# Kernel optimization log

Measured on AMD Instinct MI355X. Metric: run time of the kernel, lower is better.

The kernel has to match this reference:

```python
import jax, jax.numpy as jnp
import numpy as np

MULT = 1024
H = 16
HEAD = MULT // H  # 64

def _linear_params(key, h, out_f, in_f):
    k1, k2 = jax.random.split(key)
    bound = 1.0 / np.sqrt(in_f)
    W = jax.random.uniform(k1, (h, out_f, in_f), minval=-bound, maxval=bound, dtype=jnp.float32)
    b = jax.random.uniform(k2, (h, out_f), minval=-bound, maxval=bound, dtype=jnp.float32)
    return W, b

def setup_inputs() -> dict:
    key = jax.random.key(0)
    ks = jax.random.split(key, 6)
    t_inp = jax.random.normal(ks[0], (32768, MULT), dtype=jnp.float32)
    lat_inp = jax.random.normal(ks[1], (32768, MULT), dtype=jnp.float32)
    Wt, bt = _linear_params(ks[2], H, HEAD, MULT)
    Wl, bl = _linear_params(ks[3], H, HEAD, MULT)
    Wv, bv = _linear_params(ks[4], H, HEAD, 2 * MULT)
    k1, k2 = jax.random.split(ks[5])
    bound = 1.0 / np.sqrt(MULT)
    Wo = jax.random.uniform(k1, (MULT, MULT), minval=-bound, maxval=bound, dtype=jnp.float32)
    bo = jax.random.uniform(k2, (MULT,), minval=-bound, maxval=bound, dtype=jnp.float32)
    return {"t_inp": t_inp, "lat_inp": lat_inp, "Wt": Wt, "bt": bt,
            "Wl": Wl, "bl": bl, "Wv": Wv, "bv": bv, "Wo": Wo, "bo": bo}

def _parallel_linear(x, W, b):
    # x: [N, in], W: [H, out, in], b: [H, out] -> [N, out, H] (matches torch.stack dim=2)
    return jnp.einsum('ni,hoi->noh', x, W) + b.T[None, :, :]

def reference(t_inp, lat_inp, Wt, bt, Wl, bl, Wv, bv, Wo, bo):
    t_embed = _parallel_linear(t_inp, Wt, bt)                         # [N, HEAD, H]
    lat_emb = _parallel_linear(lat_inp, Wl, bl)                        # [N, HEAD, H]
    value_emb = _parallel_linear(jnp.concatenate((t_inp, lat_inp), axis=1), Wv, bv)  # [N, HEAD, H]
    att_weights = jax.nn.softmax(t_embed * lat_emb, axis=1)            # softmax over HEAD dim (dim=1)
    merged = (att_weights * value_emb).reshape(t_inp.shape)            # [N, MULT]
    return merged @ Wo.T + bo
```

## Files before the change

### kernel.cpp

```cpp
#include <hip/hip_runtime.h>
#include <stdint.h>
#include <stddef.h>


typedef _Float16 h8 __attribute__((ext_vector_type(8)));
typedef _Float16 h4 __attribute__((ext_vector_type(4)));
typedef float    f4 __attribute__((ext_vector_type(4)));

#define NROWS 32768

__device__ __forceinline__ void async_ld16(const void* g, void* s) {
  __builtin_amdgcn_global_load_lds(
      (const __attribute__((address_space(1))) uint32_t*)g,
      (__attribute__((address_space(3))) uint32_t*)s, 16, 0, 0);
}

#define MEMFENCE asm volatile("" ::: "memory")

template<int NT, int MODE>
__launch_bounds__(512, 2)
__global__ void gemm256(const _Float16* __restrict__ A, int lda,
                        const _Float16* __restrict__ B, int ldb,
                        const float* __restrict__ bias,
                        const _Float16* __restrict__ Et,
                        const _Float16* __restrict__ El,
                        _Float16* __restrict__ C16,
                        float* __restrict__ C32) {
  __shared__ char smem[131072];

  const int b  = blockIdx.x;
  const int bp = ((b & 7) << 6) | (b >> 3);
  const int row0 = (bp & 127) << 8;
  const int col0 = (bp >> 7) << 8;

  const int tid  = threadIdx.x;
  const int w    = tid >> 6;
  const int lane = tid & 63;
  const int quad = lane >> 4;
  const int l16  = lane & 15;
  const int wr   = w >> 2;
  const int wc   = w & 3;
  const int m    = l16 & 7;

  const uint32_t sw = (uint32_t)((quad ^ m) << 4);
  const uint32_t a0 = (uint32_t)(((wr << 7) + l16) << 7) + sw;
  const uint32_t b0 = 32768u + (uint32_t)(((wc << 6) + l16) << 7) + sw;

  const int grow = (w << 3) + (lane >> 3);
  const int ss   = ((lane & 7) ^ (lane >> 3)) << 3;
  const _Float16* pA[2][2];
  const _Float16* pB[2][2];
#pragma unroll
  for (int h = 0; h < 2; ++h)
#pragma unroll
    for (int q = 0; q < 2; ++q) {
      pA[h][q] = A + (size_t)(row0 + h * 128 + q * 64 + grow) * (size_t)lda + ss;
      pB[h][q] = B + (size_t)(col0 + h * 128 + q * 64 + grow) * (size_t)ldb + ss;
    }

  f4 acc[8][4];
  const f4 z = {0.f, 0.f, 0.f, 0.f};
#pragma unroll
  for (int i = 0; i < 8; ++i)
#pragma unroll
    for (int j = 0; j < 4; ++j) acc[i][j] = z;

  char* const sm = smem;
  const int woff = w << 10;

#pragma unroll
  for (int h = 0; h < 2; ++h)
#pragma unroll
    for (int q = 0; q < 2; ++q)
      async_ld16(pA[h][q], sm + h * 16384 + q * 8192 + woff);
#pragma unroll
  for (int h = 0; h < 2; ++h)
#pragma unroll
    for (int q = 0; q < 2; ++q)
      async_ld16(pB[h][q], sm + 32768 + h * 16384 + q * 8192 + woff);

  uint32_t cur = 0;
  for (int t = 0; t < NT; ++t) {
    const int tn = (t + 1 < NT) ? (t + 1) : t;
    const uint32_t nxt = cur ^ 65536u;

#pragma unroll
    for (int h = 0; h < 2; ++h)
#pragma unroll
      for (int q = 0; q < 2; ++q)
        async_ld16(pA[h][q] + tn * 64, sm + nxt + h * 16384 + q * 8192 + woff);
    asm volatile("s_waitcnt vmcnt(4)" ::: "memory");
    __builtin_amdgcn_s_barrier();
    MEMFENCE;
    {
      const uint32_t A0 = cur + a0, B0 = cur + b0;
      h8 af[8], bf[4];
#pragma unroll
      for (int i = 0; i < 8; ++i) af[i] = *(const h8*)(sm + A0 + i * 2048);
#pragma unroll
      for (int j = 0; j < 4; ++j) bf[j] = *(const h8*)(sm + B0 + j * 2048);
      __builtin_amdgcn_s_setprio(1);
#pragma unroll
      for (int i = 0; i < 8; ++i)
#pragma unroll
        for (int j = 0; j < 4; ++j)
          acc[i][j] = __builtin_amdgcn_mfma_f32_16x16x32_f16(af[i], bf[j],
                                                             acc[i][j], 0, 0, 0);
      __builtin_amdgcn_s_setprio(0);
    }
    MEMFENCE;
    __builtin_amdgcn_s_barrier();
    MEMFENCE;

#pragma unroll
    for (int h = 0; h < 2; ++h)
#pragma unroll
      for (int q = 0; q < 2; ++q)
        async_ld16(pB[h][q] + tn * 64, sm + nxt + 32768 + h * 16384 + q * 8192 + woff);
    {
      const uint32_t A1 = (cur + a0) ^ 64u, B1 = (cur + b0) ^ 64u;
      h8 af[8], bf[4];
#pragma unroll
      for (int i = 0; i < 8; ++i) af[i] = *(const h8*)(sm + A1 + i * 2048);
#pragma unroll
      for (int j = 0; j < 4; ++j) bf[j] = *(const h8*)(sm + B1 + j * 2048);
      __builtin_amdgcn_s_setprio(1);
#pragma unroll
      for (int i = 0; i < 8; ++i)
#pragma unroll
        for (int j = 0; j < 4; ++j)
          acc[i][j] = __builtin_amdgcn_mfma_f32_16x16x32_f16(af[i], bf[j],
                                                             acc[i][j], 0, 0, 0);
      __builtin_amdgcn_s_setprio(0);
    }
    MEMFENCE;
    __builtin_amdgcn_s_barrier();
    MEMFENCE;
    cur = nxt;
  }
  asm volatile("s_waitcnt vmcnt(0)" ::: "memory");

  const int cbase  = col0 + (wc << 6);
  const int rbase0 = row0 + (wr << 7) + (quad << 2);

  if constexpr (MODE == 0) {
    float bj[4];
#pragma unroll
    for (int j = 0; j < 4; ++j) bj[j] = bias[cbase + j * 16 + l16];
#pragma unroll
    for (int i = 0; i < 8; ++i)
#pragma unroll
      for (int j = 0; j < 4; ++j) {
        const size_t co = (size_t)(cbase + j * 16 + l16);
#pragma unroll
        for (int r = 0; r < 4; ++r)
          C16[(size_t)(rbase0 + i * 16 + r) * 1024 + co] =
              (_Float16)(acc[i][j][r] + bj[j]);
      }
  } else if constexpr (MODE == 2) {
    float bj[4];
#pragma unroll
    for (int j = 0; j < 4; ++j) bj[j] = bias[cbase + j * 16 + l16];
#pragma unroll
    for (int i = 0; i < 8; ++i)
#pragma unroll
      for (int j = 0; j < 4; ++j) {
        const size_t co = (size_t)(cbase + j * 16 + l16);
#pragma unroll
        for (int r = 0; r < 4; ++r)
          C32[(size_t)(rbase0 + i * 16 + r) * 1024 + co] = acc[i][j][r] + bj[j];
      }
  } else {
    float bvj[4];
#pragma unroll
    for (int j = 0; j < 4; ++j) bvj[j] = bias[cbase + j * 16 + l16];
#pragma unroll
    for (int i = 0; i < 8; ++i) {
      float pv[4][4];
      float s[4] = {0.f, 0.f, 0.f, 0.f};
      const int rb = rbase0 + i * 16;
#pragma unroll
      for (int j = 0; j < 4; ++j) {
        const size_t co = (size_t)(cbase + j * 16 + l16);
#pragma unroll
        for (int r = 0; r < 4; ++r) {
          const size_t off = (size_t)(rb + r) * 1024 + co;
          const float tv = (float)Et[off];
          const float lv = (float)El[off];
          const float p  = __expf(tv * lv);
          pv[j][r] = p * (acc[i][j][r] + bvj[j]);
          s[r] += p;
        }
      }
#pragma unroll
      for (int r = 0; r < 4; ++r) {
        s[r] += __shfl_xor(s[r], 1);
        s[r] += __shfl_xor(s[r], 2);
        s[r] += __shfl_xor(s[r], 4);
        s[r] += __shfl_xor(s[r], 8);
        s[r] = 1.0f / s[r];
      }
#pragma unroll
      for (int j = 0; j < 4; ++j) {
        const size_t co = (size_t)(cbase + j * 16 + l16);
#pragma unroll
        for (int r = 0; r < 4; ++r)
          C16[(size_t)(rb + r) * 1024 + co] = (_Float16)(pv[j][r] * s[r]);
      }
    }
  }
}

__global__ void cvt_inputs(const float4* __restrict__ t,
                           const float4* __restrict__ l,
                           h4* __restrict__ X) {
  const size_t idx = (size_t)blockIdx.x * 256 + threadIdx.x;
  const size_t n  = idx >> 8;
  const size_t k4 = idx & 255;
  const float4 a = t[idx];
  const float4 b = l[idx];
  h4 ha, hb;
  ha[0] = (_Float16)a.x; ha[1] = (_Float16)a.y;
  ha[2] = (_Float16)a.z; ha[3] = (_Float16)a.w;
  hb[0] = (_Float16)b.x; hb[1] = (_Float16)b.y;
  hb[2] = (_Float16)b.z; hb[3] = (_Float16)b.w;
  X[n * 512 + k4]       = ha;
  X[n * 512 + 256 + k4] = hb;
}

__global__ void cvt_flat(const float4* __restrict__ W, h4* __restrict__ Wp) {
  const int idx = blockIdx.x * 256 + threadIdx.x;
  const float4 v = W[idx];
  h4 hv;
  hv[0] = (_Float16)v.x; hv[1] = (_Float16)v.y;
  hv[2] = (_Float16)v.z; hv[3] = (_Float16)v.w;
  Wp[idx] = hv;
}

__global__ void cvt_wo_perm(const float* __restrict__ Wo,
                            _Float16* __restrict__ Wp) {
  const int idx = blockIdx.x * 256 + threadIdx.x;
  const int j = idx >> 10, c = idx & 1023;
  const int k = (c & 63) * 16 + (c >> 6);
  Wp[idx] = (_Float16)Wo[j * 1024 + k];
}

extern "C" void kernel_launch(void* const* d_in, const int* in_sizes, int n_in,
                              void* d_out, int out_size, void* d_ws, size_t ws_size,
                              hipStream_t stream) {
  const float* t_inp = (const float*)d_in[0];
  const float* l_inp = (const float*)d_in[1];
  const float* Wt = (const float*)d_in[2];
  const float* bt = (const float*)d_in[3];
  const float* Wl = (const float*)d_in[4];
  const float* bl = (const float*)d_in[5];
  const float* Wv = (const float*)d_in[6];
  const float* bv = (const float*)d_in[7];
  const float* Wo = (const float*)d_in[8];
  const float* bo = (const float*)d_in[9];
  float* out = (float*)d_out;

  char* ws = (char*)d_ws;
  _Float16* X16  = (_Float16*)ws;
  _Float16* Wt16 = (_Float16*)(ws + 134217728ull);
  _Float16* Wl16 = Wt16 + 1024 * 1024;
  _Float16* Wv16 = Wl16 + 1024 * 1024;
  _Float16* Wo16 = Wv16 + 1024 * 2048;
  _Float16* Mg   = Wo16 + 1024 * 1024;

  _Float16* Et16 = (_Float16*)d_out;
  _Float16* El16 = Et16 + (size_t)NROWS * 1024;

  cvt_inputs<<<dim3(32768), dim3(256), 0, stream>>>(
      (const float4*)t_inp, (const float4*)l_inp, (h4*)X16);
  cvt_flat<<<dim3(1024), dim3(256), 0, stream>>>((const float4*)Wt, (h4*)Wt16);
  cvt_flat<<<dim3(1024), dim3(256), 0, stream>>>((const float4*)Wl, (h4*)Wl16);
  cvt_flat<<<dim3(2048), dim3(256), 0, stream>>>((const float4*)Wv, (h4*)Wv16);
  cvt_wo_perm<<<dim3(4096), dim3(256), 0, stream>>>(Wo, Wo16);

  gemm256<16, 0><<<dim3(512), dim3(512), 0, stream>>>(
      X16, 2048, Wt16, 1024, bt, nullptr, nullptr, Et16, nullptr);
  gemm256<16, 0><<<dim3(512), dim3(512), 0, stream>>>(
      X16 + 1024, 2048, Wl16, 1024, bl, nullptr, nullptr, El16, nullptr);
  gemm256<32, 1><<<dim3(512), dim3(512), 0, stream>>>(
      X16, 2048, Wv16, 2048, bv, Et16, El16, Mg, nullptr);
  gemm256<16, 2><<<dim3(512), dim3(512), 0, stream>>>(
      Mg, 1024, Wo16, 1024, bo, nullptr, nullptr, nullptr, out);
}
```

Measured before the change: 751.2 us.

## Switch GEMM mainloop to 4-stage K=32 pipeline with unswizzled LDS layout

Restructures the GEMM main loop from a double-buffered K=64 scheme with split A/B loads into a 4-slot ring of K=32 stages, keeping three stages of async global-to-LDS loads in flight. NT doubles at every launch so each step covers half the K depth. The XOR swizzle on the LDS layout is dropped in favour of a plain 64-byte row stride. This is meant to hide global memory latency better, but it may add LDS bank conflicts and puts two barriers on every smaller K step.

```diff
diff --git a/kernel.cpp b/kernel.cpp
--- a/kernel.cpp
+++ b/kernel.cpp
@@ -16,6 +16,36 @@
 }
 
 #define MEMFENCE asm volatile("" ::: "memory")
+
+#define STAGE(slot, t)                                                        \
+  {                                                                           \
+    char* dA_ = smem + (slot) * 32768 + sdst;                                 \
+    _Pragma("unroll") for (int l_ = 0; l_ < 2; ++l_) {                        \
+      async_ld16(gA[l_] + (size_t)(t) * 32, dA_ + l_ * 8192);                 \
+      async_ld16(gB[l_] + (size_t)(t) * 32, dA_ + 16384 + l_ * 8192);         \
+    }                                                                         \
+  }
+
+#define PHASE(slot)                                                           \
+  {                                                                           \
+    __builtin_amdgcn_s_barrier();                                             \
+    MEMFENCE;                                                                 \
+    const char* As_ = smem + (slot) * 32768;                                  \
+    h8 af[8], bf[4];                                                          \
+    _Pragma("unroll") for (int i = 0; i < 8; ++i)                             \
+        af[i] = *(const h8*)(As_ + aoff + i * 1024);                          \
+    _Pragma("unroll") for (int j = 0; j < 4; ++j)                             \
+        bf[j] = *(const h8*)(As_ + boff + j * 1024);                          \
+    __builtin_amdgcn_s_setprio(1);                                            \
+    _Pragma("unroll") for (int i = 0; i < 8; ++i)                             \
+      _Pragma("unroll") for (int j = 0; j < 4; ++j)                           \
+        acc[i][j] = __builtin_amdgcn_mfma_f32_16x16x32_f16(af[i], bf[j],      \
+                                                           acc[i][j], 0, 0, 0); \
+    __builtin_amdgcn_s_setprio(0);                                            \
+    MEMFENCE;                                                                 \
+    __builtin_amdgcn_s_barrier();                                             \
+    MEMFENCE;                                                                 \
+  }
 
 template<int NT, int MODE>
 __launch_bounds__(512, 2)
@@ -40,23 +70,20 @@
   const int l16  = lane & 15;
   const int wr   = w >> 2;
   const int wc   = w & 3;
-  const int m    = l16 & 7;
-
-  const uint32_t sw = (uint32_t)((quad ^ m) << 4);
-  const uint32_t a0 = (uint32_t)(((wr << 7) + l16) << 7) + sw;
-  const uint32_t b0 = 32768u + (uint32_t)(((wc << 6) + l16) << 7) + sw;
-
-  const int grow = (w << 3) + (lane >> 3);
-  const int ss   = ((lane & 7) ^ (lane >> 3)) << 3;
-  const _Float16* pA[2][2];
-  const _Float16* pB[2][2];
-#pragma unroll
-  for (int h = 0; h < 2; ++h)
-#pragma unroll
-    for (int q = 0; q < 2; ++q) {
-      pA[h][q] = A + (size_t)(row0 + h * 128 + q * 64 + grow) * (size_t)lda + ss;
-      pB[h][q] = B + (size_t)(col0 + h * 128 + q * 64 + grow) * (size_t)ldb + ss;
-    }
+
+  const int srow = w * 16 + (lane >> 2);
+  const int schk = (lane & 3) * 8;
+  const _Float16* gA[2];
+  const _Float16* gB[2];
+#pragma unroll
+  for (int l = 0; l < 2; ++l) {
+    gA[l] = A + (size_t)(row0 + l * 128 + srow) * (size_t)lda + schk;
+    gB[l] = B + (size_t)(col0 + l * 128 + srow) * (size_t)ldb + schk;
+  }
+  const int sdst = w * 1024;
+
+  const uint32_t aoff = (uint32_t)((wr * 128 + l16) * 64 + quad * 16);
+  const uint32_t boff = (uint32_t)(16384 + (wc * 64 + l16) * 64 + quad * 16);
 
   f4 acc[8][4];
   const f4 z = {0.f, 0.f, 0.f, 0.f};
@@ -65,80 +92,21 @@
 #pragma unroll
     for (int j = 0; j < 4; ++j) acc[i][j] = z;
 
-  char* const sm = smem;
-  const int woff = w << 10;
-
-#pragma unroll
-  for (int h = 0; h < 2; ++h)
-#pragma unroll
-    for (int q = 0; q < 2; ++q)
-      async_ld16(pA[h][q], sm + h * 16384 + q * 8192 + woff);
-#pragma unroll
-  for (int h = 0; h < 2; ++h)
-#pragma unroll
-    for (int q = 0; q < 2; ++q)
-      async_ld16(pB[h][q], sm + 32768 + h * 16384 + q * 8192 + woff);
-
-  uint32_t cur = 0;
-  for (int t = 0; t < NT; ++t) {
-    const int tn = (t + 1 < NT) ? (t + 1) : t;
-    const uint32_t nxt = cur ^ 65536u;
-
-#pragma unroll
-    for (int h = 0; h < 2; ++h)
-#pragma unroll
-      for (int q = 0; q < 2; ++q)
-        async_ld16(pA[h][q] + tn * 64, sm + nxt + h * 16384 + q * 8192 + woff);
-    asm volatile("s_waitcnt vmcnt(4)" ::: "memory");
-    __builtin_amdgcn_s_barrier();
-    MEMFENCE;
-    {
-      const uint32_t A0 = cur + a0, B0 = cur + b0;
-      h8 af[8], bf[4];
-#pragma unroll
-      for (int i = 0; i < 8; ++i) af[i] = *(const h8*)(sm + A0 + i * 2048);
-#pragma unroll
-      for (int j = 0; j < 4; ++j) bf[j] = *(const h8*)(sm + B0 + j * 2048);
-      __builtin_amdgcn_s_setprio(1);
-#pragma unroll
-      for (int i = 0; i < 8; ++i)
-#pragma unroll
-        for (int j = 0; j < 4; ++j)
-          acc[i][j] = __builtin_amdgcn_mfma_f32_16x16x32_f16(af[i], bf[j],
-                                                             acc[i][j], 0, 0, 0);
-      __builtin_amdgcn_s_setprio(0);
-    }
-    MEMFENCE;
-    __builtin_amdgcn_s_barrier();
-    MEMFENCE;
-
-#pragma unroll
-    for (int h = 0; h < 2; ++h)
-#pragma unroll
-      for (int q = 0; q < 2; ++q)
-        async_ld16(pB[h][q] + tn * 64, sm + nxt + 32768 + h * 16384 + q * 8192 + woff);
-    {
-      const uint32_t A1 = (cur + a0) ^ 64u, B1 = (cur + b0) ^ 64u;
-      h8 af[8], bf[4];
-#pragma unroll
-      for (int i = 0; i < 8; ++i) af[i] = *(const h8*)(sm + A1 + i * 2048);
-#pragma unroll
-      for (int j = 0; j < 4; ++j) bf[j] = *(const h8*)(sm + B1 + j * 2048);
-      __builtin_amdgcn_s_setprio(1);
-#pragma unroll
-      for (int i = 0; i < 8; ++i)
-#pragma unroll
-        for (int j = 0; j < 4; ++j)
-          acc[i][j] = __builtin_amdgcn_mfma_f32_16x16x32_f16(af[i], bf[j],
-                                                             acc[i][j], 0, 0, 0);
-      __builtin_amdgcn_s_setprio(0);
-    }
-    MEMFENCE;
-    __builtin_amdgcn_s_barrier();
-    MEMFENCE;
-    cur = nxt;
-  }
+  STAGE(0, 0);
+  STAGE(1, 1);
+  STAGE(2, 2);
+
+  for (int t = 0; t < NT - 3; ++t) {
+    STAGE((t + 3) & 3, t + 3);
+    asm volatile("s_waitcnt vmcnt(12)" ::: "memory");
+    PHASE(t & 3);
+  }
+  asm volatile("s_waitcnt vmcnt(8)" ::: "memory");
+  PHASE((NT - 3) & 3);
+  asm volatile("s_waitcnt vmcnt(4)" ::: "memory");
+  PHASE((NT - 2) & 3);
   asm volatile("s_waitcnt vmcnt(0)" ::: "memory");
+  PHASE((NT - 1) & 3);
 
   const int cbase  = col0 + (wc << 6);
   const int rbase0 = row0 + (wr << 7) + (quad << 2);
@@ -278,12 +246,12 @@
   cvt_flat<<<dim3(2048), dim3(256), 0, stream>>>((const float4*)Wv, (h4*)Wv16);
   cvt_wo_perm<<<dim3(4096), dim3(256), 0, stream>>>(Wo, Wo16);
 
-  gemm256<16, 0><<<dim3(512), dim3(512), 0, stream>>>(
+  gemm256<32, 0><<<dim3(512), dim3(512), 0, stream>>>(
       X16, 2048, Wt16, 1024, bt, nullptr, nullptr, Et16, nullptr);
-  gemm256<16, 0><<<dim3(512), dim3(512), 0, stream>>>(
+  gemm256<32, 0><<<dim3(512), dim3(512), 0, stream>>>(
       X16 + 1024, 2048, Wl16, 1024, bl, nullptr, nullptr, El16, nullptr);
-  gemm256<32, 1><<<dim3(512), dim3(512), 0, stream>>>(
+  gemm256<64, 1><<<dim3(512), dim3(512), 0, stream>>>(
       X16, 2048, Wv16, 2048, bv, Et16, El16, Mg, nullptr);
-  gemm256<16, 2><<<dim3(512), dim3(512), 0, stream>>>(
+  gemm256<32, 2><<<dim3(512), dim3(512), 0, stream>>>(
       Mg, 1024, Wo16, 1024, bo, nullptr, nullptr, nullptr, out);
 }
```

Measured after the change: 802.1 us. +6.8%, slower.

## Restructure GEMM main loop into four-phase pipeline with staggered A/B prefetch

Applied to the files above, without the earlier changes.

Rewrites the K-loop of the 256x256 MFMA GEMM into four sub-phases, each issuing a quarter of the global-to-LDS loads interleaved with a 16-MFMA block. B tiles are prefetched two iterations ahead into the current buffer and A tiles one ahead into the next buffer. B fragments are held in registers for both k-halves while A fragments are reloaded per half. The aim is smoother overlap of memory traffic with MFMA work and lower register pressure from A fragments. The cost is twice as many barriers per iteration and a buffer-reuse scheme whose correctness depends on careful waitcnt placement.

```diff
diff --git a/kernel.cpp b/kernel.cpp
--- a/kernel.cpp
+++ b/kernel.cpp
@@ -16,6 +16,34 @@
 }
 
 #define MEMFENCE asm volatile("" ::: "memory")
+
+#define STAGE_A(hh, t, bufb)                                                  \
+  {                                                                           \
+    _Pragma("unroll") for (int q_ = 0; q_ < 2; ++q_)                          \
+        async_ld16(pA[hh][q_] + (size_t)(t) * 64,                             \
+                   smem + (bufb) + (hh) * 16384 + q_ * 8192 + woff);          \
+  }
+#define STAGE_B(hh, t, bufb)                                                  \
+  {                                                                           \
+    _Pragma("unroll") for (int q_ = 0; q_ < 2; ++q_)                          \
+        async_ld16(pB[hh][q_] + (size_t)(t) * 64,                             \
+                   smem + (bufb) + 32768 + (hh) * 16384 + q_ * 8192 + woff);  \
+  }
+
+#define LOAD_AF(bb, ihalf, kf)                                                \
+  _Pragma("unroll") for (int i_ = 0; i_ < 4; ++i_)                            \
+      af[i_] = *(const h8*)(smem + (bb) + (a_rd ^ ((kf) << 6)) +              \
+                            (ihalf) * 8192 + i_ * 2048);
+
+#define MFMA16(ih, bfb)                                                       \
+  __builtin_amdgcn_s_setprio(1);                                              \
+  _Pragma("unroll") for (int i_ = 0; i_ < 4; ++i_)                            \
+      _Pragma("unroll") for (int j_ = 0; j_ < 4; ++j_)                        \
+          acc[(ih) * 4 + i_][j_] = __builtin_amdgcn_mfma_f32_16x16x32_f16(    \
+              af[i_], bf[(bfb) + j_], acc[(ih) * 4 + i_][j_], 0, 0, 0);       \
+  __builtin_amdgcn_s_setprio(0);
+
+#define BAR  MEMFENCE; __builtin_amdgcn_s_barrier(); MEMFENCE
 
 template<int NT, int MODE>
 __launch_bounds__(512, 2)
@@ -40,14 +68,9 @@
   const int l16  = lane & 15;
   const int wr   = w >> 2;
   const int wc   = w & 3;
-  const int m    = l16 & 7;
-
-  const uint32_t sw = (uint32_t)((quad ^ m) << 4);
-  const uint32_t a0 = (uint32_t)(((wr << 7) + l16) << 7) + sw;
-  const uint32_t b0 = 32768u + (uint32_t)(((wc << 6) + l16) << 7) + sw;
 
   const int grow = (w << 3) + (lane >> 3);
-  const int ss   = ((lane & 7) ^ (lane >> 3)) << 3;
+  const int ss   = (((lane & 7) ^ (lane >> 3)) << 3);
   const _Float16* pA[2][2];
   const _Float16* pB[2][2];
 #pragma unroll
@@ -57,6 +80,11 @@
       pA[h][q] = A + (size_t)(row0 + h * 128 + q * 64 + grow) * (size_t)lda + ss;
       pB[h][q] = B + (size_t)(col0 + h * 128 + q * 64 + grow) * (size_t)ldb + ss;
     }
+  const int woff = w << 10;
+
+  const uint32_t sw   = (uint32_t)((quad ^ (l16 & 7)) << 4);
+  const uint32_t a_rd = (uint32_t)(((wr << 7) + l16) << 7) + sw;
+  const uint32_t b_rd = 32768u + (uint32_t)(((wc << 6) + l16) << 7) + sw;
 
   f4 acc[8][4];
   const f4 z = {0.f, 0.f, 0.f, 0.f};
@@ -65,77 +93,48 @@
 #pragma unroll
     for (int j = 0; j < 4; ++j) acc[i][j] = z;
 
-  char* const sm = smem;
-  const int woff = w << 10;
-
-#pragma unroll
-  for (int h = 0; h < 2; ++h)
-#pragma unroll
-    for (int q = 0; q < 2; ++q)
-      async_ld16(pA[h][q], sm + h * 16384 + q * 8192 + woff);
-#pragma unroll
-  for (int h = 0; h < 2; ++h)
-#pragma unroll
-    for (int q = 0; q < 2; ++q)
-      async_ld16(pB[h][q], sm + 32768 + h * 16384 + q * 8192 + woff);
+  STAGE_A(0, 0, 0); STAGE_A(1, 0, 0);
+  STAGE_B(0, 0, 0); STAGE_B(1, 0, 0);
+  STAGE_B(0, 1, 65536); STAGE_B(1, 1, 65536);
+  asm volatile("s_waitcnt vmcnt(4)" ::: "memory");
+  BAR;
 
   uint32_t cur = 0;
   for (int t = 0; t < NT; ++t) {
-    const int tn = (t + 1 < NT) ? (t + 1) : t;
     const uint32_t nxt = cur ^ 65536u;
-
-#pragma unroll
-    for (int h = 0; h < 2; ++h)
-#pragma unroll
-      for (int q = 0; q < 2; ++q)
-        async_ld16(pA[h][q] + tn * 64, sm + nxt + h * 16384 + q * 8192 + woff);
+    const int tA = (t + 1 < NT) ? t + 1 : NT - 1;
+    const int tB = (t + 2 < NT) ? t + 2 : NT - 1;
+
+    h8 af[4], bf[8];
+    LOAD_AF(cur, 0, 0);
+#pragma unroll
+    for (int j = 0; j < 4; ++j) bf[j]     = *(const h8*)(smem + cur + b_rd + j * 2048);
+#pragma unroll
+    for (int j = 0; j < 4; ++j) bf[4 + j] = *(const h8*)(smem + cur + (b_rd ^ 64u) + j * 2048);
+    STAGE_A(0, tA, nxt);
+    BAR;
+    MFMA16(0, 0);
+    BAR;
+
+    LOAD_AF(cur, 1, 0);
+    STAGE_A(1, tA, nxt);
+    BAR;
+    MFMA16(1, 0);
+    BAR;
+
+    LOAD_AF(cur, 0, 1);
+    STAGE_B(0, tB, cur);
+    BAR;
+    MFMA16(0, 4);
+    BAR;
+
+    LOAD_AF(cur, 1, 1);
+    STAGE_B(1, tB, cur);
     asm volatile("s_waitcnt vmcnt(4)" ::: "memory");
-    __builtin_amdgcn_s_barrier();
-    MEMFENCE;
-    {
-      const uint32_t A0 = cur + a0, B0 = cur + b0;
-      h8 af[8], bf[4];
-#pragma unroll
-      for (int i = 0; i < 8; ++i) af[i] = *(const h8*)(sm + A0 + i * 2048);
-#pragma unroll
-      for (int j = 0; j < 4; ++j) bf[j] = *(const h8*)(sm + B0 + j * 2048);
-      __builtin_amdgcn_s_setprio(1);
-#pragma unroll
-      for (int i = 0; i < 8; ++i)
-#pragma unroll
-        for (int j = 0; j < 4; ++j)
-          acc[i][j] = __builtin_amdgcn_mfma_f32_16x16x32_f16(af[i], bf[j],
-                                                             acc[i][j], 0, 0, 0);
-      __builtin_amdgcn_s_setprio(0);
-    }
-    MEMFENCE;
-    __builtin_amdgcn_s_barrier();
-    MEMFENCE;
-
-#pragma unroll
-    for (int h = 0; h < 2; ++h)
-#pragma unroll
-      for (int q = 0; q < 2; ++q)
-        async_ld16(pB[h][q] + tn * 64, sm + nxt + 32768 + h * 16384 + q * 8192 + woff);
-    {
-      const uint32_t A1 = (cur + a0) ^ 64u, B1 = (cur + b0) ^ 64u;
-      h8 af[8], bf[4];
-#pragma unroll
-      for (int i = 0; i < 8; ++i) af[i] = *(const h8*)(sm + A1 + i * 2048);
-#pragma unroll
-      for (int j = 0; j < 4; ++j) bf[j] = *(const h8*)(sm + B1 + j * 2048);
-      __builtin_amdgcn_s_setprio(1);
-#pragma unroll
-      for (int i = 0; i < 8; ++i)
-#pragma unroll
-        for (int j = 0; j < 4; ++j)
-          acc[i][j] = __builtin_amdgcn_mfma_f32_16x16x32_f16(af[i], bf[j],
-                                                             acc[i][j], 0, 0, 0);
-      __builtin_amdgcn_s_setprio(0);
-    }
-    MEMFENCE;
-    __builtin_amdgcn_s_barrier();
-    MEMFENCE;
+    BAR;
+    MFMA16(1, 4);
+    BAR;
+
     cur = nxt;
   }
   asm volatile("s_waitcnt vmcnt(0)" ::: "memory");
```

Measured after the change: 749.2 us. Within noise of the previous version (-0.3%).
